# Kernel tuning notes

Hardware: AMD Instinct MI355X
Metric: run time of the kernel (lower is better)

## Reference

```python
import jax, jax.numpy as jnp
import numpy as np

KERNELS = (2, 4, 8, 16, 32)
DICE_EPS = 1e-6
WEIGHT = 1.0


def _projections(x):
    # x: [B, D, H, W] foreground volume. Three axis-max projections, each [B, 128, 128].
    return jnp.stack([x.max(axis=3),   # axial:    max over W -> [B, D, H]
                      x.max(axis=1),   # sagittal: max over D -> [B, H, W]
                      x.max(axis=2)],  # coronal:  max over H -> [B, D, W]
                     axis=0)           # [3, B, S, S] with S = 128


def _maxpool2d(x, k):
    # x: [3, B, S, S], non-overlapping max pool with kernel=stride=k (k divides S)
    t, b, s, _ = x.shape
    return x.reshape(t, b, s // k, k, s // k, k).max(axis=(3, 5))


def setup_inputs() -> dict:
    key = jax.random.key(0)
    k1, k2 = jax.random.split(key)
    shape = (8, 2, 128, 128, 128)
    inp = jax.random.uniform(k1, shape, dtype=jnp.float32)
    tgt = jax.random.uniform(k2, shape, dtype=jnp.float32)
    return {"input": inp, "target": tgt}


def reference(input, target):
    yh = input[:, 1]   # [B, D, H, W] foreground prediction
    yt = target[:, 1]  # [B, D, H, W] foreground target

    # ---- multi-scale topology loss ----
    P = _projections(yh)  # [3, B, 128, 128]
    G = _projections(yt)
    losses = []
    for k in KERNELS:
        Pk = _maxpool2d(P, k).sum(axis=0)  # [B, 128/k, 128/k]
        Gk = _maxpool2d(G, k).sum(axis=0)
        losses.append(jnp.abs(Gk - Pk).mean())
    topo_loss = jnp.mean(jnp.stack(losses))

    # ---- dice loss (foreground channel, squared denominator) ----
    b = yh.shape[0]
    a = yh.reshape(b, -1)
    t = yt.reshape(b, -1)
    intersection = jnp.sum(a * t, axis=1)
    denom = jnp.sum(a * a, axis=1) + jnp.sum(t * t, axis=1)
    dice_coeff = (2.0 * intersection + DICE_EPS) / denom
    dice_loss = 1.0 - dice_coeff.mean()

    return WEIGHT * topo_loss + WEIGHT * dice_loss
```

## Files before the change

kernel.cpp:

```cpp
#include <hip/hip_runtime.h>

#define S 128
#define SS (S*S)
#define B 8
#define BSS (B*SS)
#define NEG_INF (-3.402823466e+38f)

#define ACC_LOSS 0
#define ACC_DICE 8
#define PA   32
#define PBF  (PA  + 2*BSS)
#define PCF  (PBF + 2*BSS)
#define PBP  (PCF + 2*BSS)
#define PCP  (PBP + 16*BSS)
#define MEMSET_BYTES 128

__device__ __forceinline__ float4 max4(float4 a, float4 b) {
  return make_float4(fmaxf(a.x,b.x), fmaxf(a.y,b.y), fmaxf(a.z,b.z), fmaxf(a.w,b.w));
}
__device__ __forceinline__ float hmax4(float4 a) {
  return fmaxf(fmaxf(a.x,a.y), fmaxf(a.z,a.w));
}
__device__ __forceinline__ float4 shflx4(float4 v, int m) {
  return make_float4(__shfl_xor(v.x,m,64), __shfl_xor(v.y,m,64),
                     __shfl_xor(v.z,m,64), __shfl_xor(v.w,m,64));
}

__global__ __launch_bounds__(1024, 4) void proj_dice_kernel(
    const float* __restrict__ gin, const float* __restrict__ gtg,
    float* __restrict__ ws)
{
  const int jc  = blockIdx.x;
  const int ic  = blockIdx.y;
  const int b   = blockIdx.z;
  const int tid = threadIdx.x;
  const int jr  = tid >> 5;
  const int kl  = tid & 31;
  const int j   = (jc << 5) + jr;
  const int i0  = ic << 4;
  const int k0  = kl << 2;
  const int w   = tid >> 6;
  const int h   = (tid >> 5) & 1;

  const float* __restrict__ xin = gin + (size_t)(2*b + 1) * (size_t)(S*SS);
  const float* __restrict__ xtg = gtg + (size_t)(2*b + 1) * (size_t)(S*SS);

  float* paI = ws + PA + (size_t)(0*B + b)*SS;
  float* paT = ws + PA + (size_t)(1*B + b)*SS;
  float* pbI = ws + PBP + (size_t)((0*B + b)*8 + ic)*SS;
  float* pbT = ws + PBP + (size_t)((1*B + b)*8 + ic)*SS;
  float* pcI = ws + PCP + (size_t)((0*B + b)*4 + jc)*SS;
  float* pcT = ws + PCP + (size_t)((1*B + b)*4 + jc)*SS;

  __shared__ float lpc[2][4][2][16][S];
  __shared__ float dred[16][3];

  float4 pba = make_float4(NEG_INF, NEG_INF, NEG_INF, NEG_INF);
  float4 pbt = pba;
  float s_at = 0.f, s_aa = 0.f, s_tt = 0.f;

  for (int r = 0; r < 4; ++r) {
    const int par = r & 1;
    #pragma unroll
    for (int q = 0; q < 4; ++q) {
      const int i = i0 + (r << 2) + q;
      const size_t off = (size_t)i*SS + (size_t)j*S + k0;
      const float4 a = *(const float4*)(xin + off);
      const float4 t = *(const float4*)(xtg + off);

      s_at = fmaf(a.x,t.x, fmaf(a.y,t.y, fmaf(a.z,t.z, fmaf(a.w,t.w, s_at))));
      s_aa = fmaf(a.x,a.x, fmaf(a.y,a.y, fmaf(a.z,a.z, fmaf(a.w,a.w, s_aa))));
      s_tt = fmaf(t.x,t.x, fmaf(t.y,t.y, fmaf(t.z,t.z, fmaf(t.w,t.w, s_tt))));

      pba = max4(pba, a);
      pbt = max4(pbt, t);

      float rma = hmax4(a), rmt = hmax4(t);
      #pragma unroll
      for (int m = 16; m >= 1; m >>= 1) {
        rma = fmaxf(rma, __shfl_xor(rma, m, 64));
        rmt = fmaxf(rmt, __shfl_xor(rmt, m, 64));
      }
      if (kl == 0) { paI[i*S + j] = rma; paT[i*S + j] = rmt; }

      const float4 pca = max4(a, shflx4(a, 32));
      const float4 pct = max4(t, shflx4(t, 32));
      if (h == 0) {
        *(float4*)&lpc[par][q][0][w][k0] = pca;
        *(float4*)&lpc[par][q][1][w][k0] = pct;
      }
    }
    __syncthreads();
    {
      const int q  = tid >> 8;
      const int t  = (tid >> 7) & 1;
      const int k  = tid & 127;
      float m = lpc[par][q][t][0][k];
      #pragma unroll
      for (int rr = 1; rr < 16; ++rr) m = fmaxf(m, lpc[par][q][t][rr][k]);
      const int i = i0 + (r << 2) + q;
      (t ? pcT : pcI)[i*S + k] = m;
    }
  }

  *(float4*)(pbI + j*S + k0) = pba;
  *(float4*)(pbT + j*S + k0) = pbt;

  float v0 = s_at, v1 = s_aa, v2 = s_tt;
  #pragma unroll
  for (int m = 32; m >= 1; m >>= 1) {
    v0 += __shfl_xor(v0, m, 64);
    v1 += __shfl_xor(v1, m, 64);
    v2 += __shfl_xor(v2, m, 64);
  }
  if ((tid & 63) == 0) { dred[w][0] = v0; dred[w][1] = v1; dred[w][2] = v2; }
  __syncthreads();
  if (tid == 0) {
    float a0 = 0.f, a1 = 0.f, a2 = 0.f;
    #pragma unroll
    for (int rr = 0; rr < 16; ++rr) { a0 += dred[rr][0]; a1 += dred[rr][1]; a2 += dred[rr][2]; }
    atomicAdd(ws + ACC_DICE + b*3 + 0, a0);
    atomicAdd(ws + ACC_DICE + b*3 + 1, a1);
    atomicAdd(ws + ACC_DICE + b*3 + 2, a2);
  }
}

__global__ __launch_bounds__(256) void reduce_maps_kernel(float* __restrict__ ws)
{
  const int g = blockIdx.x * 256 + threadIdx.x;
  if (g < 65536) {
    const int vb  = g >> 12;
    const int rem = g & 4095;
    const float4* src = (const float4*)(ws + PBP) + (size_t)vb*8*(SS/4) + rem;
    float4 m = src[0];
    #pragma unroll
    for (int p = 1; p < 8; ++p) m = max4(m, src[(size_t)p*(SS/4)]);
    ((float4*)(ws + PBF))[(size_t)vb*(SS/4) + rem] = m;
  } else {
    const int g2  = g - 65536;
    const int vb  = g2 >> 12;
    const int rem = g2 & 4095;
    const float4* src = (const float4*)(ws + PCP) + (size_t)vb*4*(SS/4) + rem;
    float4 m = src[0];
    #pragma unroll
    for (int p = 1; p < 4; ++p) m = max4(m, src[(size_t)p*(SS/4)]);
    ((float4*)(ws + PCF))[(size_t)vb*(SS/4) + rem] = m;
  }
}

__global__ __launch_bounds__(256) void pool_loss_kernel(float* __restrict__ ws)
{
  const int b   = blockIdx.x;
  const int tid = threadIdx.x;
  const int tr  = tid >> 4;
  const int tc  = tid & 15;
  const int r0  = tr << 3;
  const int c0  = tc << 3;

  float s2[2][4][4];
  float s4[2][2][2];
  float s8[2], s16[2], s32[2];
  #pragma unroll
  for (int v = 0; v < 2; ++v) {
    #pragma unroll
    for (int y = 0; y < 4; ++y)
      #pragma unroll
      for (int x = 0; x < 4; ++x) s2[v][y][x] = 0.f;
    #pragma unroll
    for (int y = 0; y < 2; ++y)
      #pragma unroll
      for (int x = 0; x < 2; ++x) s4[v][y][x] = 0.f;
    s8[v] = 0.f; s16[v] = 0.f; s32[v] = 0.f;
  }

  #pragma unroll
  for (int t = 0; t < 3; ++t) {
    #pragma unroll
    for (int vol = 0; vol < 2; ++vol) {
      const size_t region = (t == 0) ? PA : (t == 1) ? PBF : PCF;
      const float* m = ws + region + (size_t)(vol*B + b)*SS;
      float tile[8][8];
      #pragma unroll
      for (int r = 0; r < 8; ++r) {
        const float4 a = *(const float4*)(m + (size_t)(r0 + r)*S + c0);
        const float4 c = *(const float4*)(m + (size_t)(r0 + r)*S + c0 + 4);
        tile[r][0]=a.x; tile[r][1]=a.y; tile[r][2]=a.z; tile[r][3]=a.w;
        tile[r][4]=c.x; tile[r][5]=c.y; tile[r][6]=c.z; tile[r][7]=c.w;
      }
      float m2[4][4];
      #pragma unroll
      for (int y = 0; y < 4; ++y)
        #pragma unroll
        for (int x = 0; x < 4; ++x) {
          m2[y][x] = fmaxf(fmaxf(tile[2*y][2*x], tile[2*y][2*x+1]),
                           fmaxf(tile[2*y+1][2*x], tile[2*y+1][2*x+1]));
          s2[vol][y][x] += m2[y][x];
        }
      float m4[2][2];
      #pragma unroll
      for (int y = 0; y < 2; ++y)
        #pragma unroll
        for (int x = 0; x < 2; ++x) {
          m4[y][x] = fmaxf(fmaxf(m2[2*y][2*x], m2[2*y][2*x+1]),
                           fmaxf(m2[2*y+1][2*x], m2[2*y+1][2*x+1]));
          s4[vol][y][x] += m4[y][x];
        }
      float m8 = fmaxf(fmaxf(m4[0][0], m4[0][1]), fmaxf(m4[1][0], m4[1][1]));
      s8[vol] += m8;
      float m16 = m8;
      m16 = fmaxf(m16, __shfl_xor(m16, 1, 64));
      m16 = fmaxf(m16, __shfl_xor(m16, 16, 64));
      s16[vol] += m16;
      float m32 = m16;
      m32 = fmaxf(m32, __shfl_xor(m32, 2, 64));
      m32 = fmaxf(m32, __shfl_xor(m32, 32, 64));
      s32[vol] += m32;
    }
  }

  const float w0 = 1.f/(5.f*8.f*64.f*64.f);
  const float w1 = 1.f/(5.f*8.f*32.f*32.f);
  const float w2 = 1.f/(5.f*8.f*16.f*16.f);
  const float w3 = 1.f/(5.f*8.f*8.f*8.f);
  const float w4 = 1.f/(5.f*8.f*4.f*4.f);

  float l0 = 0.f;
  #pragma unroll
  for (int y = 0; y < 4; ++y)
    #pragma unroll
    for (int x = 0; x < 4; ++x) l0 += fabsf(s2[1][y][x] - s2[0][y][x]);
  float l1 = 0.f;
  #pragma unroll
  for (int y = 0; y < 2; ++y)
    #pragma unroll
    for (int x = 0; x < 2; ++x) l1 += fabsf(s4[1][y][x] - s4[0][y][x]);
  float part = l0*w0 + l1*w1 + fabsf(s8[1] - s8[0])*w2;
  if ((tid & 0x11) == 0) part += fabsf(s16[1] - s16[0])*w3;
  if ((tid & 0x33) == 0) part += fabsf(s32[1] - s32[0])*w4;

  #pragma unroll
  for (int m = 32; m >= 1; m >>= 1) part += __shfl_xor(part, m, 64);
  __shared__ float red[4];
  const int wid = tid >> 6;
  if ((tid & 63) == 0) red[wid] = part;
  __syncthreads();
  if (tid == 0) atomicAdd(ws + ACC_LOSS, red[0] + red[1] + red[2] + red[3]);
}

__global__ void finalize_kernel(const float* __restrict__ ws, float* __restrict__ out)
{
  if (threadIdx.x == 0) {
    float dsum = 0.f;
    for (int b = 0; b < B; ++b) {
      const float at = ws[ACC_DICE + b*3 + 0];
      const float aa = ws[ACC_DICE + b*3 + 1];
      const float tt = ws[ACC_DICE + b*3 + 2];
      dsum += (2.f*at + 1e-6f) / (aa + tt);
    }
    out[0] = ws[ACC_LOSS] + (1.f - dsum / (float)B);
  }
}

extern "C" void kernel_launch(void* const* d_in, const int* in_sizes, int n_in,
                              void* d_out, int out_size, void* d_ws, size_t ws_size,
                              hipStream_t stream)
{
  const float* gin = (const float*)d_in[0];
  const float* gtg = (const float*)d_in[1];
  float* ws  = (float*)d_ws;
  float* out = (float*)d_out;

  hipMemsetAsync(d_ws, 0, MEMSET_BYTES, stream);

  dim3 g1(4, 8, B);
  proj_dice_kernel<<<g1, dim3(1024), 0, stream>>>(gin, gtg, ws);

  reduce_maps_kernel<<<512, dim3(256), 0, stream>>>(ws);

  pool_loss_kernel<<<B, dim3(256), 0, stream>>>(ws);

  finalize_kernel<<<1, 64, 0, stream>>>(ws, out);
}
```

Measured before the change: 53.02 us.

## Double proj block count, drop memset and atomics via per-block partial sums

After: 56.78 us. +7.1%, slower.

```diff
diff --git a/kernel.cpp b/kernel.cpp
--- a/kernel.cpp
+++ b/kernel.cpp
@@ -8,12 +8,11 @@
 
 #define ACC_LOSS 0
 #define ACC_DICE 8
-#define PA   32
+#define PA   2048
 #define PBF  (PA  + 2*BSS)
 #define PCF  (PBF + 2*BSS)
 #define PBP  (PCF + 2*BSS)
-#define PCP  (PBP + 16*BSS)
-#define MEMSET_BYTES 128
+#define PCP  (PBP + 2*8*16*SS)
 
 __device__ __forceinline__ float4 max4(float4 a, float4 b) {
   return make_float4(fmaxf(a.x,b.x), fmaxf(a.y,b.y), fmaxf(a.z,b.z), fmaxf(a.w,b.w));
@@ -26,7 +25,7 @@
                      __shfl_xor(v.z,m,64), __shfl_xor(v.w,m,64));
 }
 
-__global__ __launch_bounds__(1024, 4) void proj_dice_kernel(
+__global__ __launch_bounds__(1024, 8) void proj_dice_kernel(
     const float* __restrict__ gin, const float* __restrict__ gtg,
     float* __restrict__ ws)
 {
@@ -37,7 +36,7 @@
   const int jr  = tid >> 5;
   const int kl  = tid & 31;
   const int j   = (jc << 5) + jr;
-  const int i0  = ic << 4;
+  const int i0  = ic << 3;
   const int k0  = kl << 2;
   const int w   = tid >> 6;
   const int h   = (tid >> 5) & 1;
@@ -47,20 +46,19 @@
 
   float* paI = ws + PA + (size_t)(0*B + b)*SS;
   float* paT = ws + PA + (size_t)(1*B + b)*SS;
-  float* pbI = ws + PBP + (size_t)((0*B + b)*8 + ic)*SS;
-  float* pbT = ws + PBP + (size_t)((1*B + b)*8 + ic)*SS;
+  float* pbI = ws + PBP + (size_t)((0*B + b)*16 + ic)*SS;
+  float* pbT = ws + PBP + (size_t)((1*B + b)*16 + ic)*SS;
   float* pcI = ws + PCP + (size_t)((0*B + b)*4 + jc)*SS;
   float* pcT = ws + PCP + (size_t)((1*B + b)*4 + jc)*SS;
 
-  __shared__ float lpc[2][4][2][16][S];
+  __shared__ float lpc[4][2][16][S];
   __shared__ float dred[16][3];
 
   float4 pba = make_float4(NEG_INF, NEG_INF, NEG_INF, NEG_INF);
   float4 pbt = pba;
   float s_at = 0.f, s_aa = 0.f, s_tt = 0.f;
 
-  for (int r = 0; r < 4; ++r) {
-    const int par = r & 1;
+  for (int r = 0; r < 2; ++r) {
     #pragma unroll
     for (int q = 0; q < 4; ++q) {
       const int i = i0 + (r << 2) + q;
@@ -86,8 +84,8 @@
       const float4 pca = max4(a, shflx4(a, 32));
       const float4 pct = max4(t, shflx4(t, 32));
       if (h == 0) {
-        *(float4*)&lpc[par][q][0][w][k0] = pca;
-        *(float4*)&lpc[par][q][1][w][k0] = pct;
+        *(float4*)&lpc[q][0][w][k0] = pca;
+        *(float4*)&lpc[q][1][w][k0] = pct;
       }
     }
     __syncthreads();
@@ -95,12 +93,13 @@
       const int q  = tid >> 8;
       const int t  = (tid >> 7) & 1;
       const int k  = tid & 127;
-      float m = lpc[par][q][t][0][k];
-      #pragma unroll
-      for (int rr = 1; rr < 16; ++rr) m = fmaxf(m, lpc[par][q][t][rr][k]);
+      float m = lpc[q][t][0][k];
+      #pragma unroll
+      for (int rr = 1; rr < 16; ++rr) m = fmaxf(m, lpc[q][t][rr][k]);
       const int i = i0 + (r << 2) + q;
       (t ? pcT : pcI)[i*S + k] = m;
     }
+    if (r == 0) __syncthreads();
   }
 
   *(float4*)(pbI + j*S + k0) = pba;
@@ -119,9 +118,10 @@
     float a0 = 0.f, a1 = 0.f, a2 = 0.f;
     #pragma unroll
     for (int rr = 0; rr < 16; ++rr) { a0 += dred[rr][0]; a1 += dred[rr][1]; a2 += dred[rr][2]; }
-    atomicAdd(ws + ACC_DICE + b*3 + 0, a0);
-    atomicAdd(ws + ACC_DICE + b*3 + 1, a1);
-    atomicAdd(ws + ACC_DICE + b*3 + 2, a2);
+    const int bid = jc + 4*ic + 64*b;
+    ws[ACC_DICE + bid*3 + 0] = a0;
+    ws[ACC_DICE + bid*3 + 1] = a1;
+    ws[ACC_DICE + bid*3 + 2] = a2;
   }
 }
 
@@ -131,10 +131,10 @@
   if (g < 65536) {
     const int vb  = g >> 12;
     const int rem = g & 4095;
-    const float4* src = (const float4*)(ws + PBP) + (size_t)vb*8*(SS/4) + rem;
+    const float4* src = (const float4*)(ws + PBP) + (size_t)vb*16*(SS/4) + rem;
     float4 m = src[0];
     #pragma unroll
-    for (int p = 1; p < 8; ++p) m = max4(m, src[(size_t)p*(SS/4)]);
+    for (int p = 1; p < 16; ++p) m = max4(m, src[(size_t)p*(SS/4)]);
     ((float4*)(ws + PBF))[(size_t)vb*(SS/4) + rem] = m;
   } else {
     const int g2  = g - 65536;
@@ -244,20 +244,32 @@
   const int wid = tid >> 6;
   if ((tid & 63) == 0) red[wid] = part;
   __syncthreads();
-  if (tid == 0) atomicAdd(ws + ACC_LOSS, red[0] + red[1] + red[2] + red[3]);
-}
-
-__global__ void finalize_kernel(const float* __restrict__ ws, float* __restrict__ out)
-{
-  if (threadIdx.x == 0) {
-    float dsum = 0.f;
-    for (int b = 0; b < B; ++b) {
-      const float at = ws[ACC_DICE + b*3 + 0];
-      const float aa = ws[ACC_DICE + b*3 + 1];
-      const float tt = ws[ACC_DICE + b*3 + 2];
-      dsum += (2.f*at + 1e-6f) / (aa + tt);
-    }
-    out[0] = ws[ACC_LOSS] + (1.f - dsum / (float)B);
+  if (tid == 0) ws[ACC_LOSS + b] = red[0] + red[1] + red[2] + red[3];
+}
+
+__global__ __launch_bounds__(512) void finalize_kernel(
+    const float* __restrict__ ws, float* __restrict__ out)
+{
+  const int tid = threadIdx.x;
+  const int w = tid >> 6;
+  __shared__ float fd[8];
+
+  float v0 = ws[ACC_DICE + tid*3 + 0];
+  float v1 = ws[ACC_DICE + tid*3 + 1];
+  float v2 = ws[ACC_DICE + tid*3 + 2];
+  #pragma unroll
+  for (int m = 32; m >= 1; m >>= 1) {
+    v0 += __shfl_xor(v0, m, 64);
+    v1 += __shfl_xor(v1, m, 64);
+    v2 += __shfl_xor(v2, m, 64);
+  }
+  if ((tid & 63) == 0) fd[w] = (2.f*v0 + 1e-6f) / (v1 + v2);
+  __syncthreads();
+  if (tid == 0) {
+    float topo = 0.f, dsum = 0.f;
+    #pragma unroll
+    for (int b = 0; b < B; ++b) { topo += ws[ACC_LOSS + b]; dsum += fd[b]; }
+    out[0] = topo + (1.f - dsum / (float)B);
   }
 }
 
@@ -270,14 +282,12 @@
   float* ws  = (float*)d_ws;
   float* out = (float*)d_out;
 
-  hipMemsetAsync(d_ws, 0, MEMSET_BYTES, stream);
-
-  dim3 g1(4, 8, B);
+  dim3 g1(4, 16, B);
   proj_dice_kernel<<<g1, dim3(1024), 0, stream>>>(gin, gtg, ws);
 
   reduce_maps_kernel<<<512, dim3(256), 0, stream>>>(ws);
 
   pool_loss_kernel<<<B, dim3(256), 0, stream>>>(ws);
 
-  finalize_kernel<<<1, 64, 0, stream>>>(ws, out);
-}
+  finalize_kernel<<<1, dim3(512), 0, stream>>>(ws, out);
+}
```
